# Kernel tuning notes

Measured on AMD Instinct MI355X. Metric: run time of the kernel, lower is better.

The kernel has to match this reference:

```python
import jax, jax.numpy as jnp
import numpy as np

NUM_HEADS = 8
NEG_SLOPE = 0.2


def setup_inputs() -> dict:
    key = jax.random.key(0)
    k1, k2, k3, k4 = jax.random.split(key, 4)
    B, N, D_IN, D_K, D_V = 4, 4096, 256, 256, 256
    x = jax.random.normal(k1, (B, N, D_IN), dtype=jnp.float32)
    Wq = jax.random.normal(k2, (D_IN, D_K), dtype=jnp.float32) * (1.0 / np.sqrt(D_IN))
    Wk = jax.random.normal(k3, (D_IN, D_K), dtype=jnp.float32) * (1.0 / np.sqrt(D_IN))
    Wv = jax.random.normal(k4, (D_IN, D_V), dtype=jnp.float32) * (1.0 / np.sqrt(D_IN))
    return {"x": x, "Wq": Wq, "Wk": Wk, "Wv": Wv}


def reference(x, Wq, Wk, Wv):
    B, N, _ = x.shape
    nh = NUM_HEADS
    dim_k = Wq.shape[1]
    dim_v = Wv.shape[1]
    dk, dv = dim_k // nh, dim_v // nh
    nor_fact = 1.0 / np.sqrt(dk)
    # project and split heads: [B, H, N, dk]
    q = (x @ Wq).reshape(B, N, nh, dk).transpose(0, 2, 1, 3)
    k = (x @ Wk).reshape(B, N, nh, dk).transpose(0, 2, 1, 3)
    v = (x @ Wv).reshape(B, N, nh, dv).transpose(0, 2, 1, 3)
    # all-pairs scores, scaled then LeakyReLU (no softmax)
    dist = jnp.einsum('bhnd,bhmd->bhnm', q, k) * nor_fact
    dist = jnp.where(dist >= 0, dist, NEG_SLOPE * dist)
    att = jnp.einsum('bhnm,bhmd->bhnd', dist, v)
    return att.transpose(0, 2, 1, 3).reshape(B, N, dim_v)
```

## Files before the change

### kernel.cpp

```cpp
#include <hip/hip_runtime.h>

typedef __attribute__((ext_vector_type(8))) short short8;
typedef __attribute__((ext_vector_type(4))) float f32x4;
typedef __attribute__((ext_vector_type(2))) float f32x2;
typedef __attribute__((ext_vector_type(2))) unsigned int u32x2;
typedef __attribute__((ext_vector_type(4))) unsigned int u32x4;

#define MFMA16x32(A, B, C) \
  __builtin_amdgcn_mfma_f32_16x16x32_bf16((A), (B), (C), 0, 0, 0)

__device__ __forceinline__ void async_cp16(const unsigned short* g, void* l) {
  __builtin_amdgcn_global_load_lds(
      (const __attribute__((address_space(1))) unsigned int*)g,
      (__attribute__((address_space(3))) unsigned int*)l, 16, 0, 0);
}

__device__ __forceinline__ unsigned int fbits(float f) {
  return __builtin_bit_cast(unsigned int, f);
}
__device__ __forceinline__ unsigned int pack_bf16(float a, float b) {
  return __builtin_amdgcn_perm(fbits(b), fbits(a), 0x07060302u);
}
__device__ __forceinline__ unsigned short bf16_rne(float f) {
  unsigned int u = fbits(f);
  return (unsigned short)((u + 0x8000u) >> 16);
}
__device__ __forceinline__ unsigned int leaky_pack(float a, float b) {
  f32x2 v = {a, b};
  f32x2 m = v * 0.2f;
  f32x2 r = __builtin_elementwise_max(v, m);
  return pack_bf16(r[0], r[1]);
}

__global__ __launch_bounds__(256) void prep_kernel(
    const float* __restrict__ x, unsigned short* __restrict__ xb,
    const float* __restrict__ Wq, const float* __restrict__ Wk,
    const float* __restrict__ Wv, unsigned short* __restrict__ WT) {
  __shared__ float tile[32][33];
  if (blockIdx.x < 4096) {
    const size_t i = ((size_t)blockIdx.x * 256 + threadIdx.x) * 4;
    const float4 f = *(const float4*)(x + i);
    u32x2 u = {(unsigned int)bf16_rne(f.x) | ((unsigned int)bf16_rne(f.y) << 16),
               (unsigned int)bf16_rne(f.z) | ((unsigned int)bf16_rne(f.w) << 16)};
    *(u32x2*)(xb + i) = u;
    return;
  }
  const int bid = blockIdx.x - 4096;
  const int g = bid / 64, rem = bid % 64;
  const int k0 = (rem >> 3) * 32, n0 = (rem & 7) * 32;
  const float* W = (g == 0) ? Wq : (g == 1) ? Wk : Wv;
  const int t = threadIdx.x;
  {
    const int kr = t >> 3, nc = (t & 7) * 4;
    const float4 f = *(const float4*)(W + (size_t)(k0 + kr) * 256 + n0 + nc);
    tile[kr][nc + 0] = f.x; tile[kr][nc + 1] = f.y;
    tile[kr][nc + 2] = f.z; tile[kr][nc + 3] = f.w;
  }
  __syncthreads();
  {
    const int nr = t >> 3, kc = (t & 7) * 4;
    unsigned int u0 = (unsigned int)bf16_rne(tile[kc + 0][nr]) |
                      ((unsigned int)bf16_rne(tile[kc + 1][nr]) << 16);
    unsigned int u1 = (unsigned int)bf16_rne(tile[kc + 2][nr]) |
                      ((unsigned int)bf16_rne(tile[kc + 3][nr]) << 16);
    u32x2 u = {u0, u1};
    *(u32x2*)(WT + (size_t)g * 65536 + (size_t)(n0 + nr) * 256 + k0 + kc) = u;
  }
}

__global__ __launch_bounds__(256, 2) void proj_kernel(
    const unsigned short* __restrict__ xb, const unsigned short* __restrict__ WT,
    unsigned short* __restrict__ QH, unsigned short* __restrict__ KH,
    unsigned short* __restrict__ VT) {
  __shared__ __align__(16) char smem[65536];
  const int tid = threadIdx.x;
  const int w = tid >> 6, lane = tid & 63, l15 = lane & 15, quad = lane >> 4;
  const int bid = blockIdx.x;
  const int mtile = bid / 6, nt = bid % 6;
  const int g = nt >> 1, n0 = (nt & 1) * 128;
  const int m0 = mtile * 128;

  const int srow = lane >> 3, useg = lane & 7;
  const int swz = (useg ^ srow) * 8;
  const unsigned short* aS = xb + (size_t)(m0 + w * 32 + srow) * 256 + swz;
  const unsigned short* bS =
      WT + (size_t)g * 65536 + (size_t)(n0 + w * 32 + srow) * 256 + swz;

#pragma unroll
  for (int j = 0; j < 4; j++) {
    async_cp16(aS + j * 2048, smem + w * 4096 + j * 1024);
    async_cp16(bS + j * 2048, smem + 16384 + w * 4096 + j * 1024);
  }
  __syncthreads();

  const f32x4 zero = {0.f, 0.f, 0.f, 0.f};
  f32x4 acc[2][8];
#pragma unroll
  for (int s = 0; s < 2; s++)
#pragma unroll
    for (int c = 0; c < 8; c++) acc[s][c] = zero;

  const int sw = l15 & 7;
  for (int t = 0; t < 4; t++) {
    const int nb = t & 1;
    const int kn = ((t + 1) & 3) * 64;
#pragma unroll
    for (int j = 0; j < 4; j++) {
      async_cp16(aS + kn + j * 2048,
                 smem + (nb ^ 1) * 32768 + w * 4096 + j * 1024);
      async_cp16(bS + kn + j * 2048,
                 smem + (nb ^ 1) * 32768 + 16384 + w * 4096 + j * 1024);
    }
    const char* Ab = smem + nb * 32768;
    const char* Bb = Ab + 16384;
#pragma unroll
    for (int ks = 0; ks < 2; ks++) {
      const int seg = ((ks * 4 + quad) ^ sw) * 16;
      short8 af[2], bf[8];
#pragma unroll
      for (int s = 0; s < 2; s++)
        af[s] = *(const short8*)(Ab + (w * 32 + s * 16 + l15) * 128 + seg);
#pragma unroll
      for (int c = 0; c < 8; c++)
        bf[c] = *(const short8*)(Bb + (c * 16 + l15) * 128 + seg);
      if (g < 2) {
#pragma unroll
        for (int s = 0; s < 2; s++)
#pragma unroll
          for (int c = 0; c < 8; c++)
            acc[s][c] = MFMA16x32(bf[c], af[s], acc[s][c]);
      } else {
#pragma unroll
        for (int s = 0; s < 2; s++)
#pragma unroll
          for (int c = 0; c < 8; c++)
            acc[s][c] = MFMA16x32(af[s], bf[c], acc[s][c]);
      }
    }
    __syncthreads();
  }

  if (g < 2) {
    unsigned short* O = g ? KH : QH;
    const float sc = g ? 1.0f : 0.17677669529663688f;
#pragma unroll
    for (int s = 0; s < 2; s++)
#pragma unroll
      for (int c = 0; c < 8; c++) {
        const int row = m0 + w * 32 + s * 16 + l15;
        const int col = n0 + c * 16 + quad * 4;
        const int bb = row >> 12, nn = row & 4095;
        const int hh = col >> 5, dl = col & 31;
        u32x2 pk = {pack_bf16(acc[s][c][0] * sc, acc[s][c][1] * sc),
                    pack_bf16(acc[s][c][2] * sc, acc[s][c][3] * sc)};
        *(u32x2*)(O + ((size_t)(bb * 8 + hh) * 4096 + nn) * 32 + dl) = pk;
      }
  } else {
#pragma unroll
    for (int s = 0; s < 2; s++)
#pragma unroll
      for (int c = 0; c < 8; c++) {
        const int col = n0 + c * 16 + l15;
        const int hh = col >> 5, dl = col & 31;
        const int row = m0 + w * 32 + s * 16 + quad * 4;
        const int bb = row >> 12;
        const int nn = (row & 4064) | (quad << 3) | ((s & 1) << 2);
        u32x2 pk = {pack_bf16(acc[s][c][0], acc[s][c][1]),
                    pack_bf16(acc[s][c][2], acc[s][c][3])};
        *(u32x2*)(VT + (size_t)((bb * 8 + hh) * 32 + dl) * 4096 + nn) = pk;
      }
  }
}

__global__ __launch_bounds__(256, 4) void attn_kernel(
    const unsigned short* __restrict__ QH, const unsigned short* __restrict__ KH,
    const unsigned short* __restrict__ VT, float* __restrict__ out) {
  __shared__ __align__(16) char smem[16384];
  const int tid = threadIdx.x;
  const int w = tid >> 6, lane = tid & 63, l15 = lane & 15, quad = lane >> 4;
  const int bid = blockIdx.x;
  const int bh = bid & 31, qh = bid >> 5;
  const int b = bh >> 3, h = bh & 7;
  const int qbase = qh * 128 + w * 32;

  const unsigned short* Qp =
      QH + ((size_t)bh * 4096 + qbase + l15) * 32 + quad * 8;
  short8 qf[2];
#pragma unroll
  for (int s = 0; s < 2; s++) qf[s] = *(const short8*)(Qp + (size_t)s * 512);

  const bool isK = (w < 2);
  const unsigned short* src0;
  size_t jstep;
  int kstr, wbOff;
  if (isK) {
    const int key = (w * 2) * 16 + (lane >> 2);
    const int gseg = (lane & 3) ^ ((lane >> 3) & 3);
    src0 = KH + ((size_t)bh * 4096 + key) * 32 + gseg * 8;
    jstep = 16 * 32;
    kstr = 32;
    wbOff = (w * 2) * 1024;
  } else {
    const int r = ((w - 2) * 2) * 8 + (lane >> 3), useg = lane & 7;
    src0 = VT + ((size_t)bh * 32 + r) * 4096 + ((useg ^ (lane >> 3)) * 8);
    jstep = (size_t)8 * 4096;
    kstr = 1;
    wbOff = 4096 + ((w - 2) * 2) * 1024;
  }

  async_cp16(src0, smem + wbOff);
  async_cp16(src0 + jstep, smem + wbOff + 1024);
  __syncthreads();

  const f32x4 zero = {0.f, 0.f, 0.f, 0.f};
  f32x4 acc[2][2];
#pragma unroll
  for (int s = 0; s < 2; s++) {
    acc[s][0] = zero;
    acc[s][1] = zero;
  }

  const int rs = l15 & 7;
  const int kseg = (quad ^ ((l15 >> 1) & 3)) * 16;
  for (int i = 0; i < 64; i++) {
    const int nb = i & 1;
    const int kn = ((i + 1) & 63) * 64;
    const unsigned short* sn = src0 + (size_t)kn * kstr;
    async_cp16(sn, smem + (nb ^ 1) * 8192 + wbOff);
    async_cp16(sn + jstep, smem + (nb ^ 1) * 8192 + wbOff + 1024);

    const char* Kb = smem + nb * 8192;
    const char* Vb = Kb + 4096;
    short8 kf[4];
#pragma unroll
    for (int c = 0; c < 4; c++)
      kf[c] = *(const short8*)(Kb + (c * 16 + l15) * 64 + kseg);
    short8 vf[2][2];
#pragma unroll
    for (int dt = 0; dt < 2; dt++) {
      const char* Vr = Vb + (dt * 16 + l15) * 128;
#pragma unroll
      for (int u = 0; u < 2; u++)
        vf[dt][u] = *(const short8*)(Vr + (((4 * u + quad) ^ rs) * 16));
    }

#pragma unroll
    for (int s = 0; s < 2; s++) {
      unsigned int pp[4][2];
#pragma unroll
      for (int c = 0; c < 4; c++) {
        f32x4 st = MFMA16x32(kf[c], qf[s], zero);
        pp[c][0] = leaky_pack(st[0], st[1]);
        pp[c][1] = leaky_pack(st[2], st[3]);
      }
#pragma unroll
      for (int u = 0; u < 2; u++) {
        u32x4 bw = {pp[2 * u][0], pp[2 * u][1],
                    pp[2 * u + 1][0], pp[2 * u + 1][1]};
        short8 pb = __builtin_bit_cast(short8, bw);
#pragma unroll
        for (int dt = 0; dt < 2; dt++)
          acc[s][dt] = MFMA16x32(vf[dt][u], pb, acc[s][dt]);
      }
    }
    __syncthreads();
  }

#pragma unroll
  for (int s = 0; s < 2; s++)
#pragma unroll
    for (int dt = 0; dt < 2; dt++)
      *(f32x4*)(out + ((size_t)b * 4096 + qbase + s * 16 + l15) * 256 + h * 32 +
                dt * 16 + quad * 4) = acc[s][dt];
}

extern "C" void kernel_launch(void* const* d_in, const int* in_sizes, int n_in,
                              void* d_out, int out_size, void* d_ws,
                              size_t ws_size, hipStream_t stream) {
  const float* x = (const float*)d_in[0];
  const float* Wq = (const float*)d_in[1];
  const float* Wk = (const float*)d_in[2];
  const float* Wv = (const float*)d_in[3];
  float* out = (float*)d_out;

  unsigned short* ws = (unsigned short*)d_ws;
  unsigned short* QHb = ws;
  unsigned short* KHb = ws + 4194304;
  unsigned short* VTb = ws + 2 * 4194304;
  unsigned short* xbb = ws + 3 * 4194304;
  unsigned short* WTb = ws + 4 * 4194304;

  prep_kernel<<<4288, 256, 0, stream>>>(x, xbb, Wq, Wk, Wv, WTb);
  proj_kernel<<<768, 256, 0, stream>>>(xbb, WTb, QHb, KHb, VTb);
  attn_kernel<<<1024, 256, 0, stream>>>(QHb, KHb, VTb, out);
}
```

Measured before the change: 179.8 us.

## Load K/V fragments directly from global memory instead of LDS double-buffering

Removes the shared-memory staging of K and V tiles, the async global-to-LDS copies and the per-iteration block barrier. Each wave now reads its K and V MFMA fragments straight from global memory (relying on L1/L2 caching since all waves share the same K/V), with the loop unrolled by two. This drops synchronization and LDS traffic but makes every wave issue redundant global loads and exposes their latency, with no explicit prefetch.

New measurement: 263.7 us. 46.7% more time.

```diff
diff --git a/kernel.cpp b/kernel.cpp
--- a/kernel.cpp
+++ b/kernel.cpp
@@ -175,7 +175,6 @@
 __global__ __launch_bounds__(256, 4) void attn_kernel(
     const unsigned short* __restrict__ QH, const unsigned short* __restrict__ KH,
     const unsigned short* __restrict__ VT, float* __restrict__ out) {
-  __shared__ __align__(16) char smem[16384];
   const int tid = threadIdx.x;
   const int w = tid >> 6, lane = tid & 63, l15 = lane & 15, quad = lane >> 4;
   const int bid = blockIdx.x;
@@ -189,28 +188,8 @@
 #pragma unroll
   for (int s = 0; s < 2; s++) qf[s] = *(const short8*)(Qp + (size_t)s * 512);
 
-  const bool isK = (w < 2);
-  const unsigned short* src0;
-  size_t jstep;
-  int kstr, wbOff;
-  if (isK) {
-    const int key = (w * 2) * 16 + (lane >> 2);
-    const int gseg = (lane & 3) ^ ((lane >> 3) & 3);
-    src0 = KH + ((size_t)bh * 4096 + key) * 32 + gseg * 8;
-    jstep = 16 * 32;
-    kstr = 32;
-    wbOff = (w * 2) * 1024;
-  } else {
-    const int r = ((w - 2) * 2) * 8 + (lane >> 3), useg = lane & 7;
-    src0 = VT + ((size_t)bh * 32 + r) * 4096 + ((useg ^ (lane >> 3)) * 8);
-    jstep = (size_t)8 * 4096;
-    kstr = 1;
-    wbOff = 4096 + ((w - 2) * 2) * 1024;
-  }
-
-  async_cp16(src0, smem + wbOff);
-  async_cp16(src0 + jstep, smem + wbOff + 1024);
-  __syncthreads();
+  const unsigned short* Kp = KH + ((size_t)bh * 4096 + l15) * 32 + quad * 8;
+  const unsigned short* Vp = VT + ((size_t)bh * 32 + l15) * 4096 + quad * 8;
 
   const f32x4 zero = {0.f, 0.f, 0.f, 0.f};
   f32x4 acc[2][2];
@@ -220,29 +199,20 @@
     acc[s][1] = zero;
   }
 
-  const int rs = l15 & 7;
-  const int kseg = (quad ^ ((l15 >> 1) & 3)) * 16;
+#pragma unroll 2
   for (int i = 0; i < 64; i++) {
-    const int nb = i & 1;
-    const int kn = ((i + 1) & 63) * 64;
-    const unsigned short* sn = src0 + (size_t)kn * kstr;
-    async_cp16(sn, smem + (nb ^ 1) * 8192 + wbOff);
-    async_cp16(sn + jstep, smem + (nb ^ 1) * 8192 + wbOff + 1024);
-
-    const char* Kb = smem + nb * 8192;
-    const char* Vb = Kb + 4096;
+    const int kbase = i * 64;
     short8 kf[4];
 #pragma unroll
     for (int c = 0; c < 4; c++)
-      kf[c] = *(const short8*)(Kb + (c * 16 + l15) * 64 + kseg);
+      kf[c] = *(const short8*)(Kp + (size_t)(kbase + c * 16) * 32);
     short8 vf[2][2];
 #pragma unroll
-    for (int dt = 0; dt < 2; dt++) {
-      const char* Vr = Vb + (dt * 16 + l15) * 128;
+    for (int dt = 0; dt < 2; dt++)
 #pragma unroll
       for (int u = 0; u < 2; u++)
-        vf[dt][u] = *(const short8*)(Vr + (((4 * u + quad) ^ rs) * 16));
-    }
+        vf[dt][u] =
+            *(const short8*)(Vp + (size_t)dt * 65536 + kbase + u * 32);
 
 #pragma unroll
     for (int s = 0; s < 2; s++) {
@@ -263,7 +233,6 @@
           acc[s][dt] = MFMA16x32(vf[dt][u], pb, acc[s][dt]);
       }
     }
-    __syncthreads();
   }
 
 #pragma unroll
```
